# Performance work log

Measured on AMD Instinct MI355X. Metric: run time of the kernel, lower is better.

## Reference

```python
import jax, jax.numpy as jnp
import numpy as np
from jax import lax
from jax.scipy.special import logsumexp

B, T, Lc = 64, 512, 16
DW, CD, NF, KS, H, K, CV = 300, 50, 100, 3, 256, 9, 100
SCALE = 0.05


def setup_inputs() -> dict:
    key = jax.random.key(0)
    ks = jax.random.split(key, 20)
    f32 = jnp.float32
    return {
        'word_embs': jax.random.normal(ks[0], (B, T, DW), f32),
        'chars': jax.random.randint(ks[1], (B, T, Lc), 0, CV),
        'lengths': jax.random.randint(ks[2], (B,), T // 2, T + 1).astype(jnp.int32),
        'tags': jax.random.randint(ks[3], (B, T), 0, K),
        'fin_W': jax.random.normal(ks[4], (DW, DW), f32) * SCALE,
        'fin_b': jnp.zeros((DW,), f32),
        'char_emb': jax.random.normal(ks[5], (CV, CD), f32) * SCALE,
        'conv_W': jax.random.normal(ks[6], (KS, CD, NF), f32) * SCALE,  # (W, In, Out)
        'conv_b': jnp.zeros((NF,), f32),
        'Wih_f': jax.random.normal(ks[7], (4 * H, DW + NF), f32) * SCALE,
        'Whh_f': jax.random.normal(ks[8], (4 * H, H), f32) * SCALE,
        'b_f': jnp.zeros((4 * H,), f32),
        'Wih_b': jax.random.normal(ks[9], (4 * H, DW + NF), f32) * SCALE,
        'Whh_b': jax.random.normal(ks[10], (4 * H, H), f32) * SCALE,
        'b_b': jnp.zeros((4 * H,), f32),
        'out_W': jax.random.normal(ks[11], (2 * H, K), f32) * SCALE,
        'out_b': jnp.zeros((K,), f32),
        'trans': jax.random.normal(ks[12], (K, K), f32) * SCALE,
        'start_trans': jax.random.normal(ks[13], (K,), f32) * SCALE,
        'end_trans': jax.random.normal(ks[14], (K,), f32) * SCALE,
    }


def _lstm_scan(x, mask, Wih, Whh, b):
    # x: [B,T,D], mask: [B,T] bool -> outputs [B,T,H] (zeros at padding)
    xT = jnp.swapaxes(x, 0, 1)              # [T,B,D]
    mT = jnp.swapaxes(mask, 0, 1)           # [T,B]
    pre = jnp.einsum('tbd,gd->tbg', xT, Wih) + b  # precompute input part [T,B,4H]
    h0 = jnp.zeros((x.shape[0], Whh.shape[1]), x.dtype)

    def step(carry, inp):
        h, c = carry
        px, m = inp
        g = px + h @ Whh.T
        i, f, gg, o = jnp.split(g, 4, axis=-1)  # pytorch gate order i,f,g,o
        c_new = jax.nn.sigmoid(f) * c + jax.nn.sigmoid(i) * jnp.tanh(gg)
        h_new = jax.nn.sigmoid(o) * jnp.tanh(c_new)
        m = m[:, None]
        h2 = jnp.where(m, h_new, h)
        c2 = jnp.where(m, c_new, c)
        return (h2, c2), h2 * m

    _, hs = lax.scan(step, (h0, h0), (pre, mT))
    return jnp.swapaxes(hs, 0, 1)


def _reverse_by_length(x, lengths):
    # reverse the valid prefix of each sequence (padding stays at the end)
    t = jnp.arange(x.shape[1])
    rev = jnp.where(t[None, :] < lengths[:, None], lengths[:, None] - 1 - t[None, :], t[None, :])
    return jnp.take_along_axis(x, rev[:, :, None], axis=1)


def _crf_forward(logits, tags, mask, trans, start_trans, end_trans):
    # torchcrf-style log-likelihood; returns scalar sum over batch
    eT = jnp.swapaxes(logits, 0, 1)  # [T,B,K]
    mT = jnp.swapaxes(mask, 0, 1).astype(logits.dtype)  # [T,B]
    bidx = jnp.arange(logits.shape[0])
    # numerator: gold path score
    score = start_trans[tags[:, 0]] + eT[0][bidx, tags[:, 0]]

    def nstep(carry, inp):
        sc, prev = carry
        e, tg, m = inp
        step_sc = trans[prev, tg] + e[bidx, tg]
        sc = sc + m * step_sc
        prev = jnp.where(m > 0, tg, prev)
        return (sc, prev), None

    tT = jnp.swapaxes(tags, 0, 1)
    (score, last_tag), _ = lax.scan(nstep, (score, tags[:, 0]), (eT[1:], tT[1:], mT[1:]))
    score = score + end_trans[last_tag]
    # denominator: log-partition via forward algorithm
    alpha = start_trans[None, :] + eT[0]

    def fstep(a, inp):
        e, m = inp
        nxt = logsumexp(a[:, :, None] + trans[None, :, :] + e[:, None, :], axis=1)
        return jnp.where(m[:, None] > 0, nxt, a), None

    alpha, _ = lax.scan(fstep, alpha, (eT[1:], mT[1:]))
    Z = logsumexp(alpha + end_trans[None, :], axis=-1)
    return jnp.sum(score - Z)


def _viterbi(logits, mask, trans, start_trans, end_trans):
    eT = jnp.swapaxes(logits, 0, 1)  # [T,B,K]
    mT = jnp.swapaxes(mask, 0, 1)    # [T,B] bool
    Ktags = logits.shape[-1]
    ident = jnp.arange(Ktags)[None, :]

    def vstep(a, inp):
        e, m = inp
        cand = a[:, :, None] + trans[None, :, :]   # [B, K_prev, K_cur]
        bp = jnp.argmax(cand, axis=1)
        nxt = jnp.max(cand, axis=1) + e
        a2 = jnp.where(m[:, None], nxt, a)
        bp = jnp.where(m[:, None], bp, ident)       # identity backptr at padding
        return a2, bp

    alpha, bps = lax.scan(vstep, start_trans[None, :] + eT[0], (eT[1:], mT[1:]))
    last = jnp.argmax(alpha + end_trans[None, :], axis=-1)

    def bstep(tag, bp):
        prev = jnp.take_along_axis(bp, tag[:, None], axis=1)[:, 0]
        return prev, tag

    tag0, tail = lax.scan(bstep, last, bps, reverse=True)  # tail[t] = tag at time t+1
    path = jnp.concatenate([tag0[:, None], jnp.swapaxes(tail, 0, 1)], axis=1)  # [B,T]
    return path * mask  # zero-pad like zero_pad(preds)


def reference(word_embs, chars, lengths, tags, fin_W, fin_b, char_emb, conv_W, conv_b,
              Wih_f, Whh_f, b_f, Wih_b, Whh_b, b_b, out_W, out_b,
              trans, start_trans, end_trans):
    mask = jnp.arange(T)[None, :] < lengths[:, None]  # [B,T]
    # 1) word embeddings through finetune linear
    we = word_embs @ fin_W.T + fin_b
    # 2) char CNN: embed -> conv1d over chars -> relu -> max-pool
    ce = char_emb[chars].reshape(B * T, Lc, CD)
    conv = lax.conv_general_dilated(ce, conv_W, (1,), 'SAME',
                                    dimension_numbers=('NWC', 'WIO', 'NWC')) + conv_b
    char_feat = jnp.max(jax.nn.relu(conv), axis=1).reshape(B, T, NF)
    # 3) concat; 4) BiLSTM (dropout=0 / eval mode)
    x = jnp.concatenate([we, char_feat], axis=-1)
    h_fwd = _lstm_scan(x, mask, Wih_f, Whh_f, b_f)
    x_rev = _reverse_by_length(x, lengths)
    h_bwd = _reverse_by_length(_lstm_scan(x_rev, mask, Wih_b, Whh_b, b_b), lengths)
    lstm_out = jnp.concatenate([h_fwd, h_bwd], axis=-1)  # [B,T,2H]
    # 5) linear head; 6-7) CRF loss + viterbi decode
    logits = lstm_out @ out_W + out_b  # [B,T,K]
    loss = -_crf_forward(logits, tags, mask, trans, start_trans, end_trans)
    preds = _viterbi(logits, mask, trans, start_trans, end_trans)
    return loss, preds
```

## Files before the change

kernel.cpp:

```cpp
#include <hip/hip_runtime.h>


__device__ __forceinline__ float sigf(float x){ return 1.0f/(1.0f + expf(-x)); }

__global__ void pack_weights(const float* __restrict__ Wih_f, const float* __restrict__ Wih_b,
                             const float* __restrict__ Whh_f, const float* __restrict__ Whh_b,
                             const float* __restrict__ fin_W,
                             float4* __restrict__ Wp_f, float4* __restrict__ Wp_b,
                             float4* __restrict__ WT_f, float4* __restrict__ WT_b,
                             float* __restrict__ finWT){
  int stride = gridDim.x*blockDim.x;
  for (int idx = blockIdx.x*blockDim.x + threadIdx.x; idx < 425872; idx += stride){
    if (idx < 204800){
      int i2 = idx; const float* W = Wih_f; float4* P = Wp_f;
      if (i2 >= 102400){ i2 -= 102400; W = Wih_b; P = Wp_b; }
      int d = i2 >> 8, j = i2 & 255;
      P[i2] = make_float4(W[j*400+d], W[(j+256)*400+d], W[(j+512)*400+d], W[(j+768)*400+d]);
    } else if (idx < 335872){
      int i2 = idx - 204800; const float* W = Whh_f; float4* P = WT_f;
      if (i2 >= 65536){ i2 -= 65536; W = Whh_b; P = WT_b; }
      int d = i2 >> 8, j = i2 & 255;
      P[i2] = make_float4(W[j*256+d], W[(j+256)*256+d], W[(j+512)*256+d], W[(j+768)*256+d]);
    } else {
      int i2 = idx - 335872;
      int d = i2 / 300, j = i2 - d*300;
      finWT[d*304 + j] = fin_W[j*300 + d];
    }
  }
}

__global__ __launch_bounds__(256) void embed_kernel(const float* __restrict__ we_in,
      const float* __restrict__ finWT, const float* __restrict__ finb, float* __restrict__ x){
  __shared__ float embT[300*16];
  int tok0 = blockIdx.x * 16;
  for (int idx = threadIdx.x; idx < 4800; idx += 256){
    int tt = idx / 300, d = idx - tt*300;
    embT[d*16 + tt] = we_in[(size_t)tok0*300 + idx];
  }
  __syncthreads();
  for (int j = threadIdx.x; j < 300; j += 256){
    float bias = finb[j];
    float acc[16];
#pragma unroll
    for (int k2=0;k2<16;k2++) acc[k2]=bias;
    const float4* e4 = (const float4*)embT;
#pragma unroll 4
    for (int d=0; d<300; d++){
      float w = finWT[d*304 + j];
      float4 a = e4[d*4+0], b2 = e4[d*4+1], c2 = e4[d*4+2], d2 = e4[d*4+3];
      acc[0]+=a.x*w;  acc[1]+=a.y*w;  acc[2]+=a.z*w;  acc[3]+=a.w*w;
      acc[4]+=b2.x*w; acc[5]+=b2.y*w; acc[6]+=b2.z*w; acc[7]+=b2.w*w;
      acc[8]+=c2.x*w; acc[9]+=c2.y*w; acc[10]+=c2.z*w;acc[11]+=c2.w*w;
      acc[12]+=d2.x*w;acc[13]+=d2.y*w;acc[14]+=d2.z*w;acc[15]+=d2.w*w;
    }
#pragma unroll
    for (int k2=0;k2<16;k2++) x[(size_t)(tok0+k2)*400 + j] = acc[k2];
  }
}

__global__ __launch_bounds__(256) void char_kernel(const int* __restrict__ chars,
      const float* __restrict__ char_emb, const float* __restrict__ convW,
      const float* __restrict__ convb, float* __restrict__ x){
  __shared__ float ce2[8*952];
  __shared__ int chs[128];
  int tok0 = blockIdx.x * 8;
  int tid = threadIdx.x;
  if (tid < 128) chs[tid] = chars[(size_t)tok0*16 + tid];
  __syncthreads();
  for (int idx = tid; idx < 7200; idx += 256){
    int tok = idx / 900; int r = idx - tok*900;
    int w1 = r / 50; int c = r - w1*50;
    float v = 0.f;
    if (w1 >= 1 && w1 <= 16) v = char_emb[chs[tok*16 + (w1-1)]*50 + c];
    ce2[tok*952 + c*19 + w1] = v;
  }
  __syncthreads();
  for (int p = tid; p < 800; p += 256){
    int tok = p / 100, f = p - tok*100;
    float s[16];
#pragma unroll
    for (int w=0; w<16; w++) s[w] = 0.f;
    const float* cebase = ce2 + tok*952;
    for (int c=0; c<50; c++){
      float cr[18];
#pragma unroll
      for (int i=0;i<18;i++) cr[i] = cebase[c*19+i];
#pragma unroll
      for (int k2=0;k2<3;k2++){
        float wv = convW[(k2*50+c)*100 + f];
#pragma unroll
        for (int w=0;w<16;w++) s[w] += cr[w+k2]*wv;
      }
    }
    float m = s[0];
#pragma unroll
    for (int w=1;w<16;w++) m = fmaxf(m, s[w]);
    m = fmaxf(0.f, m + convb[f]);
    x[(size_t)(tok0+tok)*400 + 300 + f] = m;
  }
}

__global__ __launch_bounds__(256) void pre_gemm(const float* __restrict__ x,
     const float4* __restrict__ Wp_f, const float4* __restrict__ Wp_b,
     const float* __restrict__ b_f, const float* __restrict__ b_b,
     const int* __restrict__ lengths,
     float4* __restrict__ pre_f, float4* __restrict__ pre_b,
     int t0, int log2CH){
  int dir = blockIdx.z;
  const float4* Wp = dir ? Wp_b : Wp_f;
  const float* bias = dir ? b_b : b_f;
  float4* pre = dir ? pre_b : pre_f;
  int tok0 = blockIdx.x * 64;
  int j0 = blockIdx.y * 64;
  __shared__ float As[16][68];
  __shared__ float4 Bs[4][16][16];
  __shared__ int rows_s[64];
  int tid = threadIdx.x;
  int tx = tid & 15, ty = tid >> 4;
  if (tid < 64){
    int tok = tok0 + tid;
    int b = tok >> log2CH;
    int trel = tok - (b << log2CH);
    int t = t0 + trel;
    int row;
    if (dir == 0) row = t;
    else { int len = lengths[b]; int pr = len - 1 - t; row = pr < 0 ? 0 : pr; }
    rows_s[tid] = b*512 + row;
  }
  float4 acc[4][4];
#pragma unroll
  for (int s2=0;s2<4;s2++){
    int j = j0 + tx*4 + s2;
    float4 bj = make_float4(bias[j], bias[j+256], bias[j+512], bias[j+768]);
#pragma unroll
    for (int r=0;r<4;r++) acc[r][s2] = bj;
  }
  __syncthreads();
  int tokA = tid >> 2, kqA = tid & 3;
  int jjB = tid & 63,  kbB = tid >> 6;
  float4 aReg; float4 bReg[4];
  {
    aReg = *(const float4*)&x[(size_t)rows_s[tokA]*400 + 0 + kqA*4];
#pragma unroll
    for (int rr=0;rr<4;rr++) bReg[rr] = Wp[(size_t)(0 + kbB + rr*4)*256 + j0 + jjB];
  }
  for (int kt=0; kt<25; ++kt){
    As[kqA*4+0][tokA] = aReg.x;
    As[kqA*4+1][tokA] = aReg.y;
    As[kqA*4+2][tokA] = aReg.z;
    As[kqA*4+3][tokA] = aReg.w;
#pragma unroll
    for (int rr=0;rr<4;rr++) Bs[jjB&3][kbB+rr*4][jjB>>2] = bReg[rr];
    __syncthreads();
    if (kt < 24){
      int k0n = (kt+1)*16;
      aReg = *(const float4*)&x[(size_t)rows_s[tokA]*400 + k0n + kqA*4];
#pragma unroll
      for (int rr=0;rr<4;rr++) bReg[rr] = Wp[(size_t)(k0n + kbB + rr*4)*256 + j0 + jjB];
    }
#pragma unroll
    for (int kk=0; kk<16; ++kk){
      float a[4];
#pragma unroll
      for (int r=0;r<4;r++) a[r] = As[kk][ty*4+r];
#pragma unroll
      for (int s2=0;s2<4;s2++){
        float4 b4 = Bs[s2][kk][tx];
#pragma unroll
        for (int r=0;r<4;r++){
          acc[r][s2].x += a[r]*b4.x;
          acc[r][s2].y += a[r]*b4.y;
          acc[r][s2].z += a[r]*b4.z;
          acc[r][s2].w += a[r]*b4.w;
        }
      }
    }
    __syncthreads();
  }
#pragma unroll
  for (int r=0;r<4;r++){
    int tok = tok0 + ty*4 + r;
#pragma unroll
    for (int s2=0;s2<4;s2++){
      pre[(size_t)tok*256 + j0 + tx*4 + s2] = acc[r][s2];
    }
  }
}

#define NRD 24
#define NLD 8
#define NSTREAM (64 - NRD - NLD)

__global__ __launch_bounds__(1024, 1) void lstm_scan(const float4* __restrict__ pre_f,
     const float4* __restrict__ pre_b, const float4* __restrict__ WT_f,
     const float4* __restrict__ WT_b, const int* __restrict__ lengths,
     const float* __restrict__ outW,
     float* __restrict__ logits_f, float* __restrict__ logits_b,
     float* __restrict__ st_h, float* __restrict__ st_c,
     int t0, int CH){
  int dir = blockIdx.x & 1;
  int b = blockIdx.x >> 1;
  int len = lengths[b];
  const float4* pre = (dir ? pre_b : pre_f) + (size_t)b*CH*256;
  const float4* WT = dir ? WT_b : WT_f;
  float* lg = (dir ? logits_b : logits_f) + (size_t)b*512*9;
  __shared__ float h_lds[256];
  __shared__ float4 part[3*256];
  __shared__ float oWs[2304];
  __shared__ float4 wlds[4][NLD][256];
  int tid = threadIdx.x;
  int j = tid & 255, q = tid >> 8;
  for (int i = tid; i < 2304; i += 1024) oWs[i] = outW[dir*2304 + i];
  for (int i = tid; i < 4*NLD*256; i += 1024){
    int qq = i >> 11;
    int rr = i & (NLD*256 - 1);
    int dl = rr >> 8, jj = rr & 255;
    wlds[qq][dl][jj] = WT[(size_t)(qq*64 + NRD + dl)*256 + jj];
  }
  const float4* WTq = WT + (size_t)q*64*256;
  float4 wreg[NRD];
#pragma unroll
  for (int r=0; r<NRD; ++r) wreg[r] = WTq[(size_t)r*256 + j];
  float c = 0.f;
  if (t0 == 0){
    if (tid < 256) h_lds[tid] = 0.f;
  } else {
    if (tid < 256) h_lds[tid] = st_h[(dir*64+b)*256 + tid];
    if (q == 0) c = st_c[(dir*64+b)*256 + j];
  }
  __syncthreads();
  int tend = len < t0+CH ? len : t0+CH;
  const float4* WTs = WTq + (size_t)(NRD+NLD)*256 + j;
  const float* hR = h_lds + q*64;
  const float* hL = hR + NRD;
  const float* hS = hR + NRD + NLD;
  for (int t=t0; t<tend; ++t){
    int p = dir ? (len-1-t) : t;
    float4 acc = make_float4(0.f,0.f,0.f,0.f);
#pragma unroll 8
    for (int s=0; s<NSTREAM; ++s){
      float hv = hS[s];
      float4 w = WTs[(size_t)s*256];
      acc.x += w.x*hv; acc.y += w.y*hv; acc.z += w.z*hv; acc.w += w.w*hv;
    }
#pragma unroll
    for (int r=0; r<NRD; ++r){
      float hv = hR[r];
      float4 w = wreg[r];
      acc.x += w.x*hv; acc.y += w.y*hv; acc.z += w.z*hv; acc.w += w.w*hv;
    }
#pragma unroll
    for (int l=0; l<NLD; ++l){
      float hv = hL[l];
      float4 w = wlds[q][l][j];
      acc.x += w.x*hv; acc.y += w.y*hv; acc.z += w.z*hv; acc.w += w.w*hv;
    }
    __syncthreads();
    if (q) part[(q-1)*256 + j] = acc;
    __syncthreads();
    if (q == 0){
      float4 p0 = pre[(size_t)(t - t0)*256 + j];
      float4 p1 = part[j], p2 = part[256+j], p3 = part[512+j];
      float gi = acc.x + p0.x + p1.x + p2.x + p3.x;
      float gf = acc.y + p0.y + p1.y + p2.y + p3.y;
      float gg = acc.z + p0.z + p1.z + p2.z + p3.z;
      float go = acc.w + p0.w + p1.w + p2.w + p3.w;
      c = sigf(gf)*c + sigf(gi)*tanhf(gg);
      float h = sigf(go)*tanhf(c);
      h_lds[j] = h;
    }
    __syncthreads();
    if (tid < 576){
      int k = tid >> 6, l = tid & 63;
      float s = h_lds[l]*oWs[l*9+k] + h_lds[l+64]*oWs[(l+64)*9+k]
              + h_lds[l+128]*oWs[(l+128)*9+k] + h_lds[l+192]*oWs[(l+192)*9+k];
#pragma unroll
      for (int o=32; o; o>>=1) s += __shfl_down(s, o, 64);
      if (l == 0) lg[p*9 + k] = s;
    }
  }
  if (tid < 256) st_h[(dir*64+b)*256 + tid] = h_lds[tid];
  if (q == 0) st_c[(dir*64+b)*256 + j] = c;
}

__global__ __launch_bounds__(64) void crf_viterbi_kernel(const float* __restrict__ logits_f,
     const float* __restrict__ logits_b, const float* __restrict__ outb_,
     const int* __restrict__ tags, const int* __restrict__ lengths,
     const float* __restrict__ trans, const float* __restrict__ start_trans,
     const float* __restrict__ end_trans, float* __restrict__ loss_partial,
     float* __restrict__ preds){
  int wid = blockIdx.x;
  int is_crf = wid < 64 ? 1 : 0;
  int b = is_crf ? wid : wid - 64;
  int len = lengths[b];
  int tid = threadIdx.x;
  __shared__ float e_s[4608];
  __shared__ float tr[81];
  __shared__ float alpha[9];
  __shared__ int tg[512];
  __shared__ unsigned char bp[4608];
  const float* lf = logits_f + (size_t)b*4608;
  const float* lb = logits_b + (size_t)b*4608;
  for (int i=tid; i<4608; i+=64){
    int k = i - (i/9)*9;
    e_s[i] = lf[i] + lb[i] + outb_[k];
  }
  for (int i=tid; i<81; i+=64) tr[i] = trans[i];
  if (is_crf){
    for (int i=tid; i<512; i+=64) tg[i] = tags[b*512 + i];
    __syncthreads();
    if (tid < 9) alpha[tid] = start_trans[tid] + e_s[tid];
    __syncthreads();
    for (int t=1; t<len; ++t){
      float nxt = 0.f;
      if (tid < 9){
        float v[9];
#pragma unroll
        for (int j2=0;j2<9;j2++) v[j2] = alpha[j2] + tr[j2*9+tid];
        float m = v[0];
#pragma unroll
        for (int j2=1;j2<9;j2++) m = fmaxf(m, v[j2]);
        float ssum = 0.f;
#pragma unroll
        for (int j2=0;j2<9;j2++) ssum += expf(v[j2]-m);
        nxt = m + logf(ssum) + e_s[t*9+tid];
      }
      __syncthreads();
      if (tid < 9) alpha[tid] = nxt;
      __syncthreads();
    }
    if (tid == 0){
      float m = alpha[0] + end_trans[0];
      for (int k2=1;k2<9;k2++) m = fmaxf(m, alpha[k2]+end_trans[k2]);
      float ssum = 0.f;
      for (int k2=0;k2<9;k2++) ssum += expf(alpha[k2]+end_trans[k2]-m);
      float Z = m + logf(ssum);
      int prev = tg[0];
      float sc = start_trans[prev] + e_s[prev];
      for (int t=1;t<len;++t){
        int cur = tg[t];
        sc += tr[prev*9+cur] + e_s[t*9+cur];
        prev = cur;
      }
      sc += end_trans[prev];
      loss_partial[b] = Z - sc;
    }
  } else {
    __syncthreads();
    if (tid < 9) alpha[tid] = start_trans[tid] + e_s[tid];
    __syncthreads();
    for (int t=1; t<len; ++t){
      float nxt = 0.f; int bj = 0;
      if (tid < 9){
        float m = alpha[0] + tr[tid];
#pragma unroll
        for (int j2=1;j2<9;j2++){
          float v = alpha[j2] + tr[j2*9+tid];
          if (v > m){ m = v; bj = j2; }
        }
        nxt = m + e_s[t*9+tid];
      }
      __syncthreads();
      if (tid < 9){ alpha[tid] = nxt; bp[t*9+tid] = (unsigned char)bj; }
      __syncthreads();
    }
    for (int p2 = len + tid; p2 < 512; p2 += 64) preds[(size_t)b*512 + p2] = 0.f;
    if (tid == 0){
      float m = alpha[0] + end_trans[0]; int last = 0;
      for (int k2=1;k2<9;k2++){
        float v = alpha[k2] + end_trans[k2];
        if (v > m){ m = v; last = k2; }
      }
      int cur = last;
      preds[(size_t)b*512 + (len-1)] = (float)cur;
      for (int p2 = len-2; p2 >= 0; --p2){
        cur = bp[(p2+1)*9 + cur];
        preds[(size_t)b*512 + p2] = (float)cur;
      }
    }
  }
}

__global__ void loss_sum_kernel(const float* __restrict__ lp, float* __restrict__ out){
  float v = lp[threadIdx.x];
#pragma unroll
  for (int o=32; o; o>>=1) v += __shfl_down(v, o, 64);
  if (threadIdx.x == 0) out[0] = v;
}

extern "C" void kernel_launch(void* const* d_in, const int* in_sizes, int n_in,
                              void* d_out, int out_size, void* d_ws, size_t ws_size,
                              hipStream_t stream) {
  const float* word_embs  = (const float*)d_in[0];
  const int*   chars      = (const int*)  d_in[1];
  const int*   lengths    = (const int*)  d_in[2];
  const int*   tags       = (const int*)  d_in[3];
  const float* fin_W      = (const float*)d_in[4];
  const float* fin_b      = (const float*)d_in[5];
  const float* char_emb   = (const float*)d_in[6];
  const float* conv_W     = (const float*)d_in[7];
  const float* conv_b     = (const float*)d_in[8];
  const float* Wih_f      = (const float*)d_in[9];
  const float* Whh_f      = (const float*)d_in[10];
  const float* b_f        = (const float*)d_in[11];
  const float* Wih_b      = (const float*)d_in[12];
  const float* Whh_b      = (const float*)d_in[13];
  const float* b_b        = (const float*)d_in[14];
  const float* out_W      = (const float*)d_in[15];
  const float* out_b      = (const float*)d_in[16];
  const float* trans      = (const float*)d_in[17];
  const float* start_tr   = (const float*)d_in[18];
  const float* end_tr     = (const float*)d_in[19];

  float* ws = (float*)d_ws;
  float*  x         = ws;
  float4* Wp_f      = (float4*)(ws + 13107200);
  float4* Wp_b      = (float4*)(ws + 13516800);
  float4* WT_f      = (float4*)(ws + 13926400);
  float4* WT_b      = (float4*)(ws + 14188544);
  float*  finWT     = ws + 14450688;
  float*  logits_f  = ws + 14541888;
  float*  logits_b  = ws + 14836800;
  float*  st_h      = ws + 15131712;
  float*  st_c      = ws + 15164480;
  float*  loss_part = ws + 15197248;
  const size_t FIXED_F = 15197312;
  int CH = 16, log2CH = 4;
  {
    const int cands[5]  = {512,256,128,64,32};
    const int lgs[5]    = {9,8,7,6,5};
    for (int i=0;i<5;i++){
      size_t need = (FIXED_F + (size_t)131072*cands[i]) * 4;
      if (need <= ws_size){ CH = cands[i]; log2CH = lgs[i]; break; }
    }
  }
  float4* pre_f = (float4*)(ws + FIXED_F);
  float4* pre_b = pre_f + (size_t)64*CH*256;

  float* out = (float*)d_out;

  pack_weights<<<1664, 256, 0, stream>>>(Wih_f, Wih_b, Whh_f, Whh_b, fin_W,
                                         Wp_f, Wp_b, WT_f, WT_b, finWT);
  embed_kernel<<<2048, 256, 0, stream>>>(word_embs, finWT, fin_b, x);
  char_kernel<<<4096, 256, 0, stream>>>(chars, char_emb, conv_W, conv_b, x);

  for (int t0 = 0; t0 < 512; t0 += CH){
    pre_gemm<<<dim3(CH, 4, 2), 256, 0, stream>>>(x, Wp_f, Wp_b, b_f, b_b, lengths,
                                                 pre_f, pre_b, t0, log2CH);
    lstm_scan<<<128, 1024, 0, stream>>>(pre_f, pre_b, WT_f, WT_b, lengths, out_W,
                                        logits_f, logits_b, st_h, st_c, t0, CH);
  }

  crf_viterbi_kernel<<<128, 64, 0, stream>>>(logits_f, logits_b, out_b, tags, lengths,
                                             trans, start_tr, end_tr, loss_part, out + 1);
  loss_sum_kernel<<<1, 64, 0, stream>>>(loss_part, out);
}
```

Baseline: 4.520 ms.

## Retile pre_gemm to 128-token blocks and raise lstm_scan launch-bounds occupancy hint

```diff
diff --git a/kernel.cpp b/kernel.cpp
--- a/kernel.cpp
+++ b/kernel.cpp
@@ -100,7 +100,7 @@
   }
 }
 
-__global__ __launch_bounds__(256) void pre_gemm(const float* __restrict__ x,
+__global__ __launch_bounds__(256, 2) void pre_gemm(const float* __restrict__ x,
      const float4* __restrict__ Wp_f, const float4* __restrict__ Wp_b,
      const float* __restrict__ b_f, const float* __restrict__ b_b,
      const int* __restrict__ lengths,
@@ -110,14 +110,13 @@
   const float4* Wp = dir ? Wp_b : Wp_f;
   const float* bias = dir ? b_b : b_f;
   float4* pre = dir ? pre_b : pre_f;
-  int tok0 = blockIdx.x * 64;
+  int tok0 = blockIdx.x * 128;
   int j0 = blockIdx.y * 64;
-  __shared__ float As[16][68];
-  __shared__ float4 Bs[4][16][16];
-  __shared__ int rows_s[64];
+  __shared__ float As[16][128];
+  __shared__ int rows_s[128];
   int tid = threadIdx.x;
   int tx = tid & 15, ty = tid >> 4;
-  if (tid < 64){
+  if (tid < 128){
     int tok = tok0 + tid;
     int b = tok >> log2CH;
     int trel = tok - (b << log2CH);
@@ -127,62 +126,49 @@
     else { int len = lengths[b]; int pr = len - 1 - t; row = pr < 0 ? 0 : pr; }
     rows_s[tid] = b*512 + row;
   }
-  float4 acc[4][4];
+  float4 acc[8][4];
 #pragma unroll
   for (int s2=0;s2<4;s2++){
-    int j = j0 + tx*4 + s2;
-    float4 bj = make_float4(bias[j], bias[j+256], bias[j+512], bias[j+768]);
-#pragma unroll
-    for (int r=0;r<4;r++) acc[r][s2] = bj;
-  }
+    int u = j0 + s2*16 + tx;
+    float4 bj = make_float4(bias[u], bias[u+256], bias[u+512], bias[u+768]);
+#pragma unroll
+    for (int r=0;r<8;r++) acc[r][s2] = bj;
+  }
+  int tokA = tid >> 1, khA = (tid & 1) * 8;
   __syncthreads();
-  int tokA = tid >> 2, kqA = tid & 3;
-  int jjB = tid & 63,  kbB = tid >> 6;
-  float4 aReg; float4 bReg[4];
-  {
-    aReg = *(const float4*)&x[(size_t)rows_s[tokA]*400 + 0 + kqA*4];
-#pragma unroll
-    for (int rr=0;rr<4;rr++) bReg[rr] = Wp[(size_t)(0 + kbB + rr*4)*256 + j0 + jjB];
-  }
   for (int kt=0; kt<25; ++kt){
-    As[kqA*4+0][tokA] = aReg.x;
-    As[kqA*4+1][tokA] = aReg.y;
-    As[kqA*4+2][tokA] = aReg.z;
-    As[kqA*4+3][tokA] = aReg.w;
-#pragma unroll
-    for (int rr=0;rr<4;rr++) Bs[jjB&3][kbB+rr*4][jjB>>2] = bReg[rr];
-    __syncthreads();
-    if (kt < 24){
-      int k0n = (kt+1)*16;
-      aReg = *(const float4*)&x[(size_t)rows_s[tokA]*400 + k0n + kqA*4];
-#pragma unroll
-      for (int rr=0;rr<4;rr++) bReg[rr] = Wp[(size_t)(k0n + kbB + rr*4)*256 + j0 + jjB];
-    }
-#pragma unroll
+    int k0 = kt*16;
+    {
+      const float* xr = x + (size_t)rows_s[tokA]*400 + k0 + khA;
+      float4 v0 = *(const float4*)xr;
+      float4 v1 = *(const float4*)(xr+4);
+      As[khA+0][tokA]=v0.x; As[khA+1][tokA]=v0.y; As[khA+2][tokA]=v0.z; As[khA+3][tokA]=v0.w;
+      As[khA+4][tokA]=v1.x; As[khA+5][tokA]=v1.y; As[khA+6][tokA]=v1.z; As[khA+7][tokA]=v1.w;
+    }
+    __syncthreads();
+#pragma unroll 2
     for (int kk=0; kk<16; ++kk){
-      float a[4];
-#pragma unroll
-      for (int r=0;r<4;r++) a[r] = As[kk][ty*4+r];
-#pragma unroll
-      for (int s2=0;s2<4;s2++){
-        float4 b4 = Bs[s2][kk][tx];
-#pragma unroll
-        for (int r=0;r<4;r++){
-          acc[r][s2].x += a[r]*b4.x;
-          acc[r][s2].y += a[r]*b4.y;
-          acc[r][s2].z += a[r]*b4.z;
-          acc[r][s2].w += a[r]*b4.w;
-        }
-      }
-    }
-    __syncthreads();
-  }
-#pragma unroll
-  for (int r=0;r<4;r++){
-    int tok = tok0 + ty*4 + r;
+      const float4* wrow = Wp + (size_t)(k0+kk)*256 + j0 + tx;
+      float4 b0 = wrow[0], b1 = wrow[16], b2 = wrow[32], b3 = wrow[48];
+      const float4* arow = (const float4*)&As[kk][ty*8];
+      float4 a0 = arow[0], a1 = arow[1];
+      float a[8] = {a0.x,a0.y,a0.z,a0.w,a1.x,a1.y,a1.z,a1.w};
+#pragma unroll
+      for (int r=0;r<8;r++){
+        acc[r][0].x += a[r]*b0.x; acc[r][0].y += a[r]*b0.y; acc[r][0].z += a[r]*b0.z; acc[r][0].w += a[r]*b0.w;
+        acc[r][1].x += a[r]*b1.x; acc[r][1].y += a[r]*b1.y; acc[r][1].z += a[r]*b1.z; acc[r][1].w += a[r]*b1.w;
+        acc[r][2].x += a[r]*b2.x; acc[r][2].y += a[r]*b2.y; acc[r][2].z += a[r]*b2.z; acc[r][2].w += a[r]*b2.w;
+        acc[r][3].x += a[r]*b3.x; acc[r][3].y += a[r]*b3.y; acc[r][3].z += a[r]*b3.z; acc[r][3].w += a[r]*b3.w;
+      }
+    }
+    __syncthreads();
+  }
+#pragma unroll
+  for (int r=0;r<8;r++){
+    int tok = tok0 + ty*8 + r;
 #pragma unroll
     for (int s2=0;s2<4;s2++){
-      pre[(size_t)tok*256 + j0 + tx*4 + s2] = acc[r][s2];
+      pre[(size_t)tok*256 + j0 + s2*16 + tx] = acc[r][s2];
     }
   }
 }
@@ -191,7 +177,7 @@
 #define NLD 8
 #define NSTREAM (64 - NRD - NLD)
 
-__global__ __launch_bounds__(1024, 1) void lstm_scan(const float4* __restrict__ pre_f,
+__global__ __launch_bounds__(1024, 4) void lstm_scan(const float4* __restrict__ pre_f,
      const float4* __restrict__ pre_b, const float4* __restrict__ WT_f,
      const float4* __restrict__ WT_b, const int* __restrict__ lengths,
      const float* __restrict__ outW,
@@ -445,8 +431,8 @@
   char_kernel<<<4096, 256, 0, stream>>>(chars, char_emb, conv_W, conv_b, x);
 
   for (int t0 = 0; t0 < 512; t0 += CH){
-    pre_gemm<<<dim3(CH, 4, 2), 256, 0, stream>>>(x, Wp_f, Wp_b, b_f, b_b, lengths,
-                                                 pre_f, pre_b, t0, log2CH);
+    pre_gemm<<<dim3(CH/2, 4, 2), 256, 0, stream>>>(x, Wp_f, Wp_b, b_f, b_b, lengths,
+                                                   pre_f, pre_b, t0, log2CH);
     lstm_scan<<<128, 1024, 0, stream>>>(pre_f, pre_b, WT_f, WT_b, lengths, out_W,
                                         logits_f, logits_b, st_h, st_c, t0, CH);
   }
```

After: 4.643 ms. 2.7% more time.

## Split each LSTM sequence across two workgroups exchanging hidden state via global flags

Applied to the files above, without the earlier changes.

```diff
diff --git a/kernel.cpp b/kernel.cpp
--- a/kernel.cpp
+++ b/kernel.cpp
@@ -187,57 +187,68 @@
   }
 }
 
-#define NRD 24
+__global__ void init_flags(int* __restrict__ flags){
+  flags[threadIdx.x] = 0;
+}
+
+#define NRD 12
 #define NLD 8
-#define NSTREAM (64 - NRD - NLD)
-
-__global__ __launch_bounds__(1024, 1) void lstm_scan(const float4* __restrict__ pre_f,
+#define NSTREAM (32 - NRD - NLD)
+
+__global__ __launch_bounds__(1024) void lstm_scan(const float4* __restrict__ pre_f,
      const float4* __restrict__ pre_b, const float4* __restrict__ WT_f,
      const float4* __restrict__ WT_b, const int* __restrict__ lengths,
      const float* __restrict__ outW,
      float* __restrict__ logits_f, float* __restrict__ logits_b,
      float* __restrict__ st_h, float* __restrict__ st_c,
+     float* __restrict__ hx, int* __restrict__ flags,
      int t0, int CH){
-  int dir = blockIdx.x & 1;
-  int b = blockIdx.x >> 1;
+  int wid = blockIdx.x;
+  int pair = wid & 127;
+  int gh = wid >> 7;
+  int dir = pair & 1;
+  int b = pair >> 1;
   int len = lengths[b];
   const float4* pre = (dir ? pre_b : pre_f) + (size_t)b*CH*256;
   const float4* WT = dir ? WT_b : WT_f;
   float* lg = (dir ? logits_b : logits_f) + (size_t)b*512*9;
-  __shared__ float h_lds[256];
-  __shared__ float4 part[3*256];
+  __shared__ float h_full[256];
+  __shared__ float4 part[7*128];
   __shared__ float oWs[2304];
-  __shared__ float4 wlds[4][NLD][256];
+  __shared__ float4 wlds[8][NLD][128];
   int tid = threadIdx.x;
-  int j = tid & 255, q = tid >> 8;
-  for (int i = tid; i < 2304; i += 1024) oWs[i] = outW[dir*2304 + i];
-  for (int i = tid; i < 4*NLD*256; i += 1024){
-    int qq = i >> 11;
-    int rr = i & (NLD*256 - 1);
-    int dl = rr >> 8, jj = rr & 255;
-    wlds[qq][dl][jj] = WT[(size_t)(qq*64 + NRD + dl)*256 + jj];
-  }
-  const float4* WTq = WT + (size_t)q*64*256;
+  int j2 = tid & 127, q = tid >> 7;
+  if (gh == 0){
+    for (int i = tid; i < 2304; i += 1024) oWs[i] = outW[dir*2304 + i];
+  }
+  for (int i = tid; i < 8*NLD*128; i += 1024){
+    int qq = i >> 10;
+    int rr = i & 1023;
+    int dl = rr >> 7, jj = rr & 127;
+    wlds[qq][dl][jj] = WT[(size_t)(qq*32 + NRD + dl)*256 + gh*128 + jj];
+  }
+  const float4* WTg = WT + gh*128 + j2;
   float4 wreg[NRD];
 #pragma unroll
-  for (int r=0; r<NRD; ++r) wreg[r] = WTq[(size_t)r*256 + j];
+  for (int r=0; r<NRD; ++r) wreg[r] = WTg[(size_t)(q*32 + r)*256];
   float c = 0.f;
   if (t0 == 0){
-    if (tid < 256) h_lds[tid] = 0.f;
+    if (tid < 256) h_full[tid] = 0.f;
   } else {
-    if (tid < 256) h_lds[tid] = st_h[(dir*64+b)*256 + tid];
-    if (q == 0) c = st_c[(dir*64+b)*256 + j];
+    if (tid < 256) h_full[tid] = st_h[(dir*64+b)*256 + tid];
+    if (q == 0) c = st_c[(dir*64+b)*256 + gh*128 + j2];
   }
   __syncthreads();
   int tend = len < t0+CH ? len : t0+CH;
-  const float4* WTs = WTq + (size_t)(NRD+NLD)*256 + j;
-  const float* hR = h_lds + q*64;
+  const float4* WTs = WTg + (size_t)(q*32 + NRD + NLD)*256;
+  const float* hR = h_full + q*32;
   const float* hL = hR + NRD;
   const float* hS = hR + NRD + NLD;
   for (int t=t0; t<tend; ++t){
+    int local_t = t - t0;
     int p = dir ? (len-1-t) : t;
     float4 acc = make_float4(0.f,0.f,0.f,0.f);
-#pragma unroll 8
+#pragma unroll
     for (int s=0; s<NSTREAM; ++s){
       float hv = hS[s];
       float4 w = WTs[(size_t)s*256];
@@ -252,35 +263,48 @@
 #pragma unroll
     for (int l=0; l<NLD; ++l){
       float hv = hL[l];
-      float4 w = wlds[q][l][j];
+      float4 w = wlds[q][l][j2];
       acc.x += w.x*hv; acc.y += w.y*hv; acc.z += w.z*hv; acc.w += w.w*hv;
     }
     __syncthreads();
-    if (q) part[(q-1)*256 + j] = acc;
-    __syncthreads();
+    if (q) part[(q-1)*128 + j2] = acc;
+    __syncthreads();
+    float* hxb = hx + ((size_t)(local_t & 1)*128 + pair)*256;
     if (q == 0){
-      float4 p0 = pre[(size_t)(t - t0)*256 + j];
-      float4 p1 = part[j], p2 = part[256+j], p3 = part[512+j];
-      float gi = acc.x + p0.x + p1.x + p2.x + p3.x;
-      float gf = acc.y + p0.y + p1.y + p2.y + p3.y;
-      float gg = acc.z + p0.z + p1.z + p2.z + p3.z;
-      float go = acc.w + p0.w + p1.w + p2.w + p3.w;
+      float4 p0 = pre[(size_t)local_t*256 + gh*128 + j2];
+      float gi = acc.x + p0.x, gf = acc.y + p0.y, gg = acc.z + p0.z, go = acc.w + p0.w;
+#pragma unroll
+      for (int u=0; u<7; ++u){
+        float4 pu = part[u*128 + j2];
+        gi += pu.x; gf += pu.y; gg += pu.z; go += pu.w;
+      }
       c = sigf(gf)*c + sigf(gi)*tanhf(gg);
       float h = sigf(go)*tanhf(c);
-      h_lds[j] = h;
-    }
-    __syncthreads();
-    if (tid < 576){
+      h_full[gh*128 + j2] = h;
+      __hip_atomic_store(&hxb[gh*128 + j2], h, __ATOMIC_RELAXED, __HIP_MEMORY_SCOPE_AGENT);
+    }
+    __syncthreads();
+    if (tid == 0){
+      __hip_atomic_store(&flags[wid], local_t+1, __ATOMIC_RELEASE, __HIP_MEMORY_SCOPE_AGENT);
+      while (__hip_atomic_load(&flags[wid ^ 128], __ATOMIC_ACQUIRE, __HIP_MEMORY_SCOPE_AGENT) < local_t+1) { }
+    }
+    __syncthreads();
+    if (tid < 128){
+      h_full[(1-gh)*128 + tid] =
+        __hip_atomic_load(&hxb[(1-gh)*128 + tid], __ATOMIC_RELAXED, __HIP_MEMORY_SCOPE_AGENT);
+    }
+    __syncthreads();
+    if (gh == 0 && tid < 576){
       int k = tid >> 6, l = tid & 63;
-      float s = h_lds[l]*oWs[l*9+k] + h_lds[l+64]*oWs[(l+64)*9+k]
-              + h_lds[l+128]*oWs[(l+128)*9+k] + h_lds[l+192]*oWs[(l+192)*9+k];
+      float s = h_full[l]*oWs[l*9+k] + h_full[l+64]*oWs[(l+64)*9+k]
+              + h_full[l+128]*oWs[(l+128)*9+k] + h_full[l+192]*oWs[(l+192)*9+k];
 #pragma unroll
       for (int o=32; o; o>>=1) s += __shfl_down(s, o, 64);
       if (l == 0) lg[p*9 + k] = s;
     }
   }
-  if (tid < 256) st_h[(dir*64+b)*256 + tid] = h_lds[tid];
-  if (q == 0) st_c[(dir*64+b)*256 + j] = c;
+  if (tid < 128) st_h[(dir*64+b)*256 + gh*128 + tid] = h_full[gh*128 + tid];
+  if (q == 0) st_c[(dir*64+b)*256 + gh*128 + j2] = c;
 }
 
 __global__ __launch_bounds__(64) void crf_viterbi_kernel(const float* __restrict__ logits_f,
@@ -423,8 +447,10 @@
   float*  logits_b  = ws + 14836800;
   float*  st_h      = ws + 15131712;
   float*  st_c      = ws + 15164480;
-  float*  loss_part = ws + 15197248;
-  const size_t FIXED_F = 15197312;
+  float*  hx        = ws + 15197248;
+  int*    flags     = (int*)(ws + 15262784);
+  float*  loss_part = ws + 15263040;
+  const size_t FIXED_F = 15263104;
   int CH = 16, log2CH = 4;
   {
     const int cands[5]  = {512,256,128,64,32};
@@ -447,8 +473,9 @@
   for (int t0 = 0; t0 < 512; t0 += CH){
     pre_gemm<<<dim3(CH, 4, 2), 256, 0, stream>>>(x, Wp_f, Wp_b, b_f, b_b, lengths,
                                                  pre_f, pre_b, t0, log2CH);
-    lstm_scan<<<128, 1024, 0, stream>>>(pre_f, pre_b, WT_f, WT_b, lengths, out_W,
-                                        logits_f, logits_b, st_h, st_c, t0, CH);
+    init_flags<<<1, 256, 0, stream>>>(flags);
+    lstm_scan<<<256, 1024, 0, stream>>>(pre_f, pre_b, WT_f, WT_b, lengths, out_W,
+                                        logits_f, logits_b, st_h, st_c, hx, flags, t0, CH);
   }
 
   crf_viterbi_kernel<<<128, 64, 0, stream>>>(logits_f, logits_b, out_b, tags, lengths,
```

Result: slower. 6.386 ms (+41.3%).
